# Kernel optimization log

Measured on AMD Instinct MI355X. Metric: run time of the kernel, lower is better.

The kernel has to match this reference:

```python
import jax, jax.numpy as jnp
import numpy as np

N_LINKS = 100000
N_EDGES = 1600000
D = 64          # link_state_dim
RU = 256        # readout_units
G = 256         # number of graphs
T = 4           # message passing iterations


def _glorot(key, shape):
    fan_in, fan_out = shape[0], shape[1]
    limit = np.sqrt(6.0 / (fan_in + fan_out)).astype(np.float32)
    return jax.random.uniform(key, shape, jnp.float32, -limit, limit)


def setup_inputs() -> dict:
    key = jax.random.key(0)
    ks = jax.random.split(key, 12)
    states_action = jax.random.normal(ks[0], (N_LINKS, D), jnp.float32)
    states_graph_ids = jnp.sort(jax.random.randint(ks[1], (N_LINKS,), 0, G))
    states_first = jax.random.randint(ks[2], (N_EDGES,), 0, N_LINKS)
    states_second = jax.random.randint(ks[3], (N_EDGES,), 0, N_LINKS)
    # Message: Dense(2D -> D) with selu
    W_msg = _glorot(ks[4], (2 * D, D)); b_msg = jnp.zeros((D,), jnp.float32)
    # GCN: Linear(D -> D) + relu, then unsorted_segment_sum
    W_gcn = _glorot(ks[5], (D, D)); b_gcn = jnp.zeros((D,), jnp.float32)
    # Readout MLP: D -> RU -> RU -> 1
    W_r1 = _glorot(ks[6], (D, RU)); b_r1 = jnp.zeros((RU,), jnp.float32)
    W_r2 = _glorot(ks[7], (RU, RU)); b_r2 = jnp.zeros((RU,), jnp.float32)
    W_r3 = _glorot(ks[8], (RU, 1)); b_r3 = jnp.zeros((1,), jnp.float32)
    return {
        "states_action": states_action,
        "W_msg": W_msg, "b_msg": b_msg,
        "W_gcn": W_gcn, "b_gcn": b_gcn,
        "W_r1": W_r1, "b_r1": b_r1,
        "W_r2": W_r2, "b_r2": b_r2,
        "W_r3": W_r3, "b_r3": b_r3,
        "states_graph_ids": states_graph_ids,
        "states_first": states_first,
        "states_second": states_second,
        "sates_num_edges": N_EDGES,
    }


def reference(states_action, W_msg, b_msg, W_gcn, b_gcn,
              W_r1, b_r1, W_r2, b_r2, W_r3, b_r3,
              states_graph_ids, states_first, states_second, sates_num_edges):
    n_links = states_action.shape[0]
    link_state = states_action
    for _ in range(T):
        main_e = link_state[states_first]      # [E, D]
        neigh_e = link_state[states_second]    # [E, D]
        concat = jnp.concatenate([main_e, neigh_e], axis=1)  # [E, 2D]
        msg = jax.nn.selu(concat @ W_msg + b_msg)            # [E, D]
        h = jax.nn.relu(msg @ W_gcn + b_gcn)                 # [E, D]
        # scatter-add messages back onto links (segment ids = states_second)
        link_state = jax.ops.segment_sum(h, states_second, num_segments=n_links)
        # dropout rate is 0.0 -> identity
    # per-graph readout (graph ids are sorted, fixed G segments)
    graph_emb = jax.ops.segment_sum(link_state, states_graph_ids, num_segments=G)
    r = jax.nn.selu(graph_emb @ W_r1 + b_r1)
    r = jax.nn.selu(r @ W_r2 + b_r2)
    r = r @ W_r3 + b_r3                                      # [G, 1]
    return r
```

## Files before the change

### kernel.cpp

```cpp
#include <hip/hip_runtime.h>
#include <hip/hip_bf16.h>
#include <math.h>

#define D 64
#define RU 256
#define CHUNK 8
#define QSTRIDE 68
#define SSTRIDE 72
#define BIN_SHIFT 7
#define NSB 256

#if __has_builtin(__builtin_amdgcn_exp2f)
#define EXP2F(x) __builtin_amdgcn_exp2f(x)
#else
#define EXP2F(x) exp2f(x)
#endif

typedef short bf16x8 __attribute__((ext_vector_type(8)));
typedef float f32x4 __attribute__((ext_vector_type(4)));

__device__ __forceinline__ float selu_f(float x) {
    return x > 0.0f ? 1.0507009873554805f * x
                    : 1.7580993408473766f * (__expf(x) - 1.0f);
}

__device__ __forceinline__ float selu_x2(float x2) {
    const float p = fmaxf(x2, 0.0f);
    const float n = fminf(x2, 0.0f);
    const float e = EXP2F(n);
    return fmaf(1.7580993408473766f, e, fmaf(0.72829042516f, p, -1.7580993408473766f));
}

__device__ __forceinline__ short f2bf_rtne(float x) {
    union { float f; unsigned u; } v; v.f = x;
    unsigned r = (v.u + 0x7FFFu + ((v.u >> 16) & 1u)) >> 16;
    return (short)r;
}
__device__ __forceinline__ float bf2f(short s) {
    union { float f; unsigned u; } v; v.u = ((unsigned)(unsigned short)s) << 16;
    return v.f;
}
__device__ __forceinline__ unsigned packpair(float a, float b) {
    float2 p; p.x = a; p.y = b;
    __hip_bfloat162 hb = __float22bfloat162_rn(p);
    return *(unsigned*)&hb;
}

__device__ __forceinline__ bf16x8 pack8(const float* v) {
    union { bf16x8 v; unsigned u[4]; } H;
#pragma unroll
    for (int j = 0; j < 4; ++j) H.u[j] = packpair(v[2 * j], v[2 * j + 1]);
    return H.v;
}

#define FIDX(ks, jt, qd, m) ((((((ks) * 4 + (jt)) * 4 + (qd)) * 16) + (m)) * 8)

__global__ __launch_bounds__(256) void wprep_kernel(
    const float* __restrict__ W_msg, const float* __restrict__ W_gcn,
    unsigned short* __restrict__ WAh, unsigned short* __restrict__ WAl,
    unsigned short* __restrict__ WBh, unsigned short* __restrict__ WBl,
    unsigned short* __restrict__ WGh)
{
    const float LOG2E = 1.4426950408889634f;
    const int t = blockIdx.x * 256 + threadIdx.x;
    if (t >= 4096) return;
    const int i  = t & 7;
    const int m  = (t >> 3) & 15;
    const int qd = (t >> 7) & 3;
    const int jt = (t >> 9) & 3;
    const int ks = t >> 11;
    const int kk = ks * 32 + qd * 8 + i;
    const int nn = jt * 16 + m;

    float w = W_msg[kk * 64 + nn] * LOG2E;
    short hi = f2bf_rtne(w);
    WAh[t] = (unsigned short)hi;
    WAl[t] = (unsigned short)f2bf_rtne(w - bf2f(hi));

    w = W_msg[(64 + kk) * 64 + nn] * LOG2E;
    hi = f2bf_rtne(w);
    WBh[t] = (unsigned short)hi;
    WBl[t] = (unsigned short)f2bf_rtne(w - bf2f(hi));

    WGh[t] = (unsigned short)f2bf_rtne(W_gcn[kk * 64 + nn]);
}

__global__ __launch_bounds__(256) void s2bf_kernel(
    const float* __restrict__ in, unsigned short* __restrict__ out, int n4)
{
    for (int i = blockIdx.x * 256 + threadIdx.x; i < n4; i += gridDim.x * 256) {
        const float4 v = ((const float4*)in)[i];
        uint2 o;
        o.x = packpair(v.x, v.y);
        o.y = packpair(v.z, v.w);
        ((uint2*)out)[i] = o;
    }
}


__global__ __launch_bounds__(256) void histA_kernel(
    const int* __restrict__ second, int* __restrict__ ghist,
    int n_edges, int nbins)
{
    __shared__ int lhist[1024];
    for (int i = threadIdx.x; i < nbins; i += 256) lhist[i] = 0;
    __syncthreads();
    const int per = (n_edges + gridDim.x - 1) / gridDim.x;
    const int e0 = blockIdx.x * per;
    const int e1 = min(e0 + per, n_edges);
    for (int e = e0 + threadIdx.x; e < e1; e += 256)
        atomicAdd(&lhist[second[e] >> BIN_SHIFT], 1);
    __syncthreads();
    for (int i = threadIdx.x; i < nbins; i += 256)
        ghist[i * gridDim.x + blockIdx.x] = lhist[i];
}

__global__ __launch_bounds__(64) void sumbins_kernel(
    int* __restrict__ ghist, int* __restrict__ btot, int nbins)
{
    const int b = blockIdx.x, tid = threadIdx.x;
    int d[4], p[4];
#pragma unroll
    for (int k = 0; k < 4; ++k) {
        d[k] = ghist[b * NSB + k * 64 + tid];
        p[k] = d[k];
    }
#pragma unroll
    for (int off = 1; off < 64; off <<= 1) {
#pragma unroll
        for (int k = 0; k < 4; ++k) {
            const int t = __shfl_up(p[k], off, 64);
            if (tid >= off) p[k] += t;
        }
    }
    int base = 0;
#pragma unroll
    for (int k = 0; k < 4; ++k) {
        const int tot = __shfl(p[k], 63, 64);
        ghist[b * NSB + k * 64 + tid] = base + p[k] - d[k];
        base += tot;
    }
    if (tid == 63) btot[b] = base;
}

__global__ __launch_bounds__(1024) void scanS_kernel(int* __restrict__ data, int n)
{
    __shared__ int wsum[16], woff[16];
    const int tid = threadIdx.x, wave = tid >> 6, lane = tid & 63;
    const int x = (tid < n) ? data[tid] : 0;
    int v = x;
#pragma unroll
    for (int off = 1; off < 64; off <<= 1) {
        const int t = __shfl_up(v, off, 64);
        if (lane >= off) v += t;
    }
    if (lane == 63) wsum[wave] = v;
    __syncthreads();
    if (wave == 0) {
        int s = (lane < 16) ? wsum[lane] : 0;
#pragma unroll
        for (int off = 1; off < 16; off <<= 1) {
            const int t = __shfl_up(s, off, 64);
            if (lane >= off) s += t;
        }
        if (lane < 16) woff[lane] = s - wsum[lane];
    }
    __syncthreads();
    if (tid < n) data[tid] = woff[wave] + v - x;
}

__global__ __launch_bounds__(256) void scatterC_kernel(
    const int* __restrict__ first, const int* __restrict__ second,
    const int* __restrict__ ghist, const int* __restrict__ btot,
    unsigned* __restrict__ tmp, int n_edges, int nbins)
{
    __shared__ int lcur[1024];
    for (int i = threadIdx.x; i < nbins; i += 256)
        lcur[i] = ghist[i * NSB + blockIdx.x] + btot[i];
    __syncthreads();
    const int per = (n_edges + gridDim.x - 1) / gridDim.x;
    const int e0 = blockIdx.x * per;
    const int e1 = min(e0 + per, n_edges);
    for (int e = e0 + threadIdx.x; e < e1; e += 256) {
        const int s = second[e];
        const int pos = atomicAdd(&lcur[s >> BIN_SHIFT], 1);
        tmp[pos] = (unsigned)first[e] | ((unsigned)(s & 127) << 20);
    }
}

__global__ __launch_bounds__(256) void binsortD_kernel(
    const unsigned* __restrict__ tmp, const int* __restrict__ btot,
    int* __restrict__ sfirst, int* __restrict__ row_ptr,
    int n_edges, int n_links, int nbins)
{
    __shared__ int ldeg[128];
    __shared__ int lpre[128];
    __shared__ int lcur[128];
    const int b = blockIdx.x;
    const int tid = threadIdx.x;
    const int lbase = b << BIN_SHIFT;
    const int nl = min(128, n_links - lbase);
    const int eb = btot[b];
    const int ee = (b + 1 < nbins) ? btot[b + 1] : n_edges;

    if (tid < 128) ldeg[tid] = 0;
    __syncthreads();
    for (int e = eb + tid; e < ee; e += 256)
        atomicAdd(&ldeg[tmp[e] >> 20], 1);
    __syncthreads();
    if (tid < 64) {
        const int d0 = ldeg[tid], d1 = ldeg[64 + tid];
        int p0 = d0, p1 = d1;
#pragma unroll
        for (int off = 1; off < 64; off <<= 1) {
            const int t0 = __shfl_up(p0, off, 64);
            const int t1 = __shfl_up(p1, off, 64);
            if (tid >= off) { p0 += t0; p1 += t1; }
        }
        const int tot0 = __shfl(p0, 63, 64);
        lpre[tid] = p0 - d0;
        lpre[64 + tid] = tot0 + p1 - d1;
    }
    __syncthreads();
    if (tid < nl) row_ptr[lbase + tid] = eb + lpre[tid];
    if (b == nbins - 1 && tid == 0) row_ptr[n_links] = n_edges;
    if (tid < 128) lcur[tid] = lpre[tid];
    __syncthreads();
    for (int e = eb + tid; e < ee; e += 256) {
        const unsigned v = tmp[e];
        const int pos = eb + atomicAdd(&lcur[v >> 20], 1);
        sfirst[pos] = (int)(v & 0x7FFFFFu);
    }
    if (b == 0)
        for (int i = tid; i < 64; i += 256) sfirst[n_edges + i] = 0;
}

__global__ __launch_bounds__(256) void growfind_kernel(
    const int* __restrict__ gid, int* __restrict__ grow, int n_links, int G)
{
    const int g = blockIdx.x * blockDim.x + threadIdx.x;
    if (g > G) return;
    if (g == G) { grow[G] = n_links; return; }
    int lo = 0, hi = n_links;
    while (lo < hi) {
        const int mid = (lo + hi) >> 1;
        if (gid[mid] < g) lo = mid + 1; else hi = mid;
    }
    grow[g] = lo;
}

__global__ __launch_bounds__(256) void p_mfma_kernel(
    const unsigned short* __restrict__ Sb,
    const unsigned short* __restrict__ WAh, const unsigned short* __restrict__ WAl,
    unsigned short* __restrict__ P, int n_links)
{
    const int tid = threadIdx.x;
    const int wave = tid >> 6;
    const int lane = tid & 63;
    const int m = lane & 15;
    const int qd = lane >> 4;

    bf16x8 Bh[2][4], Bl[2][4];
#pragma unroll
    for (int ks = 0; ks < 2; ++ks)
#pragma unroll
        for (int jt = 0; jt < 4; ++jt) {
            const int off = FIDX(ks, jt, qd, m);
            Bh[ks][jt] = *(const bf16x8*)(WAh + off);
            Bl[ks][jt] = *(const bf16x8*)(WAl + off);
        }
    const bf16x8 z = (bf16x8){0, 0, 0, 0, 0, 0, 0, 0};

    const int ngroups = (n_links + 63) >> 6;
    for (int g = blockIdx.x; g < ngroups; g += gridDim.x) {
        const int base = g * 64 + wave * 16;
        const int l = base + m;
        bf16x8 Ah0 = z, Ah1 = z;
        if (l < n_links) {
            Ah0 = *(const bf16x8*)(Sb + (size_t)l * D + qd * 8);
            Ah1 = *(const bf16x8*)(Sb + (size_t)l * D + 32 + qd * 8);
        }
        f32x4 accP[4];
#pragma unroll
        for (int jt = 0; jt < 4; ++jt) {
            accP[jt] = (f32x4){0.f, 0.f, 0.f, 0.f};
            accP[jt] = __builtin_amdgcn_mfma_f32_16x16x32_bf16(Ah0, Bh[0][jt], accP[jt], 0, 0, 0);
            accP[jt] = __builtin_amdgcn_mfma_f32_16x16x32_bf16(Ah0, Bl[0][jt], accP[jt], 0, 0, 0);
            accP[jt] = __builtin_amdgcn_mfma_f32_16x16x32_bf16(Ah1, Bh[1][jt], accP[jt], 0, 0, 0);
            accP[jt] = __builtin_amdgcn_mfma_f32_16x16x32_bf16(Ah1, Bl[1][jt], accP[jt], 0, 0, 0);
        }
#pragma unroll
        for (int r = 0; r < 4; ++r) {
            const int lr = base + qd * 4 + r;
            if (lr < n_links) {
#pragma unroll
                for (int jt = 0; jt < 4; ++jt)
                    P[(size_t)lr * D + jt * 16 + m] =
                        (unsigned short)f2bf_rtne(accP[jt][r]);
            }
        }
    }
}

__global__ __launch_bounds__(256, 4) void edge_link_kernel(
    unsigned short* __restrict__ Sb, const unsigned short* __restrict__ P,
    const int* __restrict__ sfirst, const int* __restrict__ row_ptr,
    const float* __restrict__ b_msg,
    const unsigned short* __restrict__ WBh, const unsigned short* __restrict__ WBl,
    const unsigned short* __restrict__ WGh,
    const float* __restrict__ b_gcn,
    const unsigned short* __restrict__ WAh, const unsigned short* __restrict__ WAl,
    unsigned short* __restrict__ Pout, int do_p,
    int n_links)
{
    __shared__ float qt[4][CHUNK * QSTRIDE + 4];
    __shared__ unsigned short srow[4][CHUNK * SSTRIDE];
    const int tid = threadIdx.x;
    const int wave = tid >> 6;
    const int lane = tid & 63;
    const int m = lane & 15;
    const int qd = lane >> 4;

    const int l0 = (blockIdx.x * 4 + wave) * CHUNK;
    if (l0 >= n_links) return;
    const int nl = min(CHUNK, n_links - l0);

    const float LOG2E = 1.4426950408889634f;
    float bmsgC[4];
#pragma unroll
    for (int jt = 0; jt < 4; ++jt) bmsgC[jt] = b_msg[jt * 16 + m] * LOG2E;

    {
        const bf16x8 z = (bf16x8){0, 0, 0, 0, 0, 0, 0, 0};
        const int l = l0 + m;
        bf16x8 Ah0 = z, Ah1 = z;
        if ((l < n_links) && (m < CHUNK)) {
            Ah0 = *(const bf16x8*)(Sb + (size_t)l * D + qd * 8);
            Ah1 = *(const bf16x8*)(Sb + (size_t)l * D + 32 + qd * 8);
        }
        f32x4 accQ[4];
#pragma unroll
        for (int jt = 0; jt < 4; ++jt) accQ[jt] = (f32x4){0.f, 0.f, 0.f, 0.f};
#pragma unroll
        for (int ks = 0; ks < 2; ++ks) {
            bf16x8 WbH[4], WbL[4];
#pragma unroll
            for (int jt = 0; jt < 4; ++jt) {
                const int off = FIDX(ks, jt, qd, m);
                WbH[jt] = *(const bf16x8*)(WBh + off);
                WbL[jt] = *(const bf16x8*)(WBl + off);
            }
            const bf16x8 A = ks ? Ah1 : Ah0;
#pragma unroll
            for (int jt = 0; jt < 4; ++jt) {
                accQ[jt] = __builtin_amdgcn_mfma_f32_16x16x32_bf16(A, WbH[jt], accQ[jt], 0, 0, 0);
                accQ[jt] = __builtin_amdgcn_mfma_f32_16x16x32_bf16(A, WbL[jt], accQ[jt], 0, 0, 0);
            }
        }
#pragma unroll
        for (int r = 0; r < 4; ++r) {
            const int row = qd * 4 + r;
            if (row < CHUNK) {
#pragma unroll
                for (int jt = 0; jt < 4; ++jt)
                    qt[wave][row * QSTRIDE + jt * 16 + m] = accQ[jt][r] + bmsgC[jt];
            }
        }
    }

    bf16x8 Gh[2][4];
#pragma unroll
    for (int ks = 0; ks < 2; ++ks)
#pragma unroll
        for (int jt = 0; jt < 4; ++jt)
            Gh[ks][jt] = *(const bf16x8*)(WGh + FIDX(ks, jt, qd, m));

    float bias_gcn[4];
#pragma unroll
    for (int jt = 0; jt < 4; ++jt) bias_gcn[jt] = b_gcn[jt * 16 + m];

    const int rpv = row_ptr[l0 + min(lane, nl)];
#define RP(i) __shfl(rpv, (i), 64)
    const int eb = __builtin_amdgcn_readfirstlane(RP(0));
    const int ee = __builtin_amdgcn_readfirstlane(RP(nl));
    if (eb >= ee) {
        for (int i = 0; i < nl; ++i) {
            Sb[(size_t)(l0 + i) * D + lane] = 0;
            if (do_p)
                __builtin_nontemporal_store((unsigned short)0,
                    &Pout[(size_t)(l0 + i) * D + lane]);
        }
        return;
    }
    const int ntiles = (ee - eb + 15) >> 4;

    int sv0 = sfirst[eb + m];
    int sv1 = sfirst[eb + 16 + m];
    bf16x8 p00, p01;
    {
        const unsigned short* Pr = P + (size_t)(sv0 & 0xFFFFF) * D;
        p00 = *(const bf16x8*)(Pr + qd * 8);
        p01 = *(const bf16x8*)(Pr + 32 + qd * 8);
    }

    int bcur = 0;
    float rsum[4] = {0.f, 0.f, 0.f, 0.f};
    int eo = eb;

    for (int t = 0; t < ntiles; ++t, eo += 16) {
        const int sv2 = sfirst[eo + 32 + m];
        const unsigned short* Pr1 = P + (size_t)(sv1 & 0xFFFFF) * D;
        const bf16x8 p10 = *(const bf16x8*)(Pr1 + qd * 8);
        const bf16x8 p11 = *(const bf16x8*)(Pr1 + 32 + qd * 8);

        const bool valid = (eo + m < ee);
        const int limv = valid ? ((sv0 >> 20) & 7) : 8;
        const int qoff = (valid ? ((sv0 >> 20) & 7) : 0) * QSTRIDE + qd * 8;

        float qb[16];
        *(float4*)&qb[0]  = *(const float4*)&qt[wave][qoff];
        *(float4*)&qb[4]  = *(const float4*)&qt[wave][qoff + 4];
        *(float4*)&qb[8]  = *(const float4*)&qt[wave][qoff + 32];
        *(float4*)&qb[12] = *(const float4*)&qt[wave][qoff + 36];

        float msgA[8];
#pragma unroll
        for (int i = 0; i < 8; ++i)
            msgA[i] = selu_x2(bf2f(p00[i]) + qb[i]);
        const bf16x8 Ah0 = pack8(msgA);
        float msgB[8];
#pragma unroll
        for (int i = 0; i < 8; ++i)
            msgB[i] = selu_x2(bf2f(p01[i]) + qb[8 + i]);
        const bf16x8 Ah1 = pack8(msgB);

        f32x4 acc[4];
#pragma unroll
        for (int jt = 0; jt < 4; ++jt) {
            const float b = bias_gcn[jt];
            acc[jt] = (f32x4){b, b, b, b};
            acc[jt] = __builtin_amdgcn_mfma_f32_16x16x32_bf16(Ah0, Gh[0][jt], acc[jt], 0, 0, 0);
            acc[jt] = __builtin_amdgcn_mfma_f32_16x16x32_bf16(Ah1, Gh[1][jt], acc[jt], 0, 0, 0);
        }

        float rel[4][4];
#pragma unroll
        for (int jt = 0; jt < 4; ++jt)
#pragma unroll
            for (int r = 0; r < 4; ++r)
                rel[jt][r] = fmaxf(acc[jt][r], 0.0f);

        const int lr0 = __shfl(limv, qd * 4 + 0, 64);
        const int lr1 = __shfl(limv, qd * 4 + 1, 64);
        const int lr2 = __shfl(limv, qd * 4 + 2, 64);
        const int lr3 = __shfl(limv, qd * 4 + 3, 64);

        while (true) {
            const int b0 = bcur;
#pragma unroll
            for (int jt = 0; jt < 4; ++jt) {
                rsum[jt] += ((lr0 == b0) ? rel[jt][0] : 0.0f)
                          + ((lr1 == b0) ? rel[jt][1] : 0.0f)
                          + ((lr2 == b0) ? rel[jt][2] : 0.0f)
                          + ((lr3 == b0) ? rel[jt][3] : 0.0f);
            }
            if (bcur < nl && RP(bcur + 1) <= eo + 16) {
#pragma unroll
                for (int jt = 0; jt < 4; ++jt) {
                    rsum[jt] += __shfl_xor(rsum[jt], 16, 64);
                    rsum[jt] += __shfl_xor(rsum[jt], 32, 64);
                }
                const float outv = (qd == 0) ? rsum[0] : (qd == 1) ? rsum[1]
                                 : (qd == 2) ? rsum[2] : rsum[3];
                const unsigned short sbv = (unsigned short)f2bf_rtne(outv);
                Sb[(size_t)(l0 + bcur) * D + lane] = sbv;
                srow[wave][bcur * SSTRIDE + lane] = sbv;
#pragma unroll
                for (int jt = 0; jt < 4; ++jt) rsum[jt] = 0.0f;
                ++bcur;
                if (bcur >= nl) break;
            } else {
                break;
            }
        }

        sv0 = sv1; sv1 = sv2;
        p00 = p10; p01 = p11;
    }

    while (bcur < nl) {
        Sb[(size_t)(l0 + bcur) * D + lane] = 0;
        srow[wave][bcur * SSTRIDE + lane] = 0;
        ++bcur;
    }

    if (do_p) {
        const bf16x8 z = (bf16x8){0, 0, 0, 0, 0, 0, 0, 0};
        bf16x8 Sa0 = z, Sa1 = z;
        if (m < nl) {
            Sa0 = *(const bf16x8*)&srow[wave][m * SSTRIDE + qd * 8];
            Sa1 = *(const bf16x8*)&srow[wave][m * SSTRIDE + 32 + qd * 8];
        }
        f32x4 accP[4];
#pragma unroll
        for (int jt = 0; jt < 4; ++jt) accP[jt] = (f32x4){0.f, 0.f, 0.f, 0.f};
#pragma unroll
        for (int ks = 0; ks < 2; ++ks) {
            const bf16x8 A = ks ? Sa1 : Sa0;
#pragma unroll
            for (int jt = 0; jt < 4; ++jt) {
                const int off = FIDX(ks, jt, qd, m);
                const bf16x8 BH = *(const bf16x8*)(WAh + off);
                const bf16x8 BL = *(const bf16x8*)(WAl + off);
                accP[jt] = __builtin_amdgcn_mfma_f32_16x16x32_bf16(A, BH, accP[jt], 0, 0, 0);
                accP[jt] = __builtin_amdgcn_mfma_f32_16x16x32_bf16(A, BL, accP[jt], 0, 0, 0);
            }
        }
#pragma unroll
        for (int r = 0; r < 4; ++r) {
            const int lr = qd * 4 + r;
            if (lr < nl) {
#pragma unroll
                for (int jt = 0; jt < 4; ++jt)
                    __builtin_nontemporal_store(
                        (unsigned short)f2bf_rtne(accP[jt][r]),
                        &Pout[(size_t)(l0 + lr) * D + jt * 16 + m]);
            }
        }
    }
#undef RP
}

__global__ __launch_bounds__(256) void gsum8_kernel(
    const unsigned short* __restrict__ Sb, const int* __restrict__ grow,
    float* __restrict__ gemb)
{
    __shared__ float red[4][64];
    const int g = blockIdx.x >> 3;
    const int slice = blockIdx.x & 7;
    const int slot = threadIdx.x >> 6;
    const int j = threadIdx.x & 63;
    const int ls = grow[g], le = grow[g + 1];
    float acc = 0.0f;
    for (int l = ls + slice * 4 + slot; l < le; l += 32)
        acc += bf2f((short)Sb[(size_t)l * D + j]);
    red[slot][j] = acc;
    __syncthreads();
    if (slot == 0)
        atomicAdd(&gemb[g * D + j], red[0][j] + red[1][j] + red[2][j] + red[3][j]);
}

__global__ __launch_bounds__(256) void mlp_kernel(
    const float* __restrict__ gemb,
    const float* __restrict__ W_r1, const float* __restrict__ b_r1,
    const float* __restrict__ W_r2, const float* __restrict__ b_r2,
    const float* __restrict__ W_r3, const float* __restrict__ b_r3,
    float* __restrict__ out)
{
    __shared__ float gl[64];
    __shared__ float row1[RU];
    __shared__ float row2[RU];
    __shared__ float fin[4];
    const int g = blockIdx.x;
    const int tid = threadIdx.x;
    const int slot = tid >> 6;
    const int lane = tid & 63;

    if (tid < 64) gl[tid] = gemb[g * D + tid];
    __syncthreads();

    float a1 = b_r1[tid];
#pragma unroll 8
    for (int k = 0; k < 64; ++k) a1 += gl[k] * W_r1[k * RU + tid];
    row1[tid] = selu_f(a1);
    __syncthreads();

    float a2 = b_r2[tid];
#pragma unroll 8
    for (int k = 0; k < RU; ++k) a2 += row1[k] * W_r2[k * RU + tid];
    row2[tid] = selu_f(a2);
    __syncthreads();

    float p = row2[tid] * W_r3[tid];
#pragma unroll
    for (int off = 32; off >= 1; off >>= 1)
        p += __shfl_down(p, off, 64);
    if (lane == 0) fin[slot] = p;
    __syncthreads();
    if (tid == 0)
        out[g] = fin[0] + fin[1] + fin[2] + fin[3] + b_r3[0];
}

extern "C" void kernel_launch(void* const* d_in, const int* in_sizes, int n_in,
                              void* d_out, int out_size, void* d_ws, size_t ws_size,
                              hipStream_t stream)
{
    const float* states_action = (const float*)d_in[0];
    const float* W_msg = (const float*)d_in[1];
    const float* b_msg = (const float*)d_in[2];
    const float* W_gcn = (const float*)d_in[3];
    const float* b_gcn = (const float*)d_in[4];
    const float* W_r1 = (const float*)d_in[5];
    const float* b_r1 = (const float*)d_in[6];
    const float* W_r2 = (const float*)d_in[7];
    const float* b_r2 = (const float*)d_in[8];
    const float* W_r3 = (const float*)d_in[9];
    const float* b_r3 = (const float*)d_in[10];
    const int* gid = (const int*)d_in[11];
    const int* first = (const int*)d_in[12];
    const int* second = (const int*)d_in[13];

    const int n_links = in_sizes[0] / D;
    const int n_edges = in_sizes[12];
    const int G = out_size;
    const int nbins = (n_links + 127) >> BIN_SHIFT;

    char* ws2 = (char*)d_ws;
    auto alloc = [&](size_t bytes) {
        char* p = ws2; ws2 += (bytes + 63) & ~(size_t)63; return p;
    };
    unsigned short* Sb = (unsigned short*)alloc((size_t)n_links * D * 2);
    unsigned short* Pb = (unsigned short*)alloc((size_t)n_links * D * 2);
    float* gemb = (float*)alloc((size_t)G * D * sizeof(float));
    int* row_ptr = (int*)alloc((size_t)(n_links + 1) * sizeof(int));
    int* grow = (int*)alloc((size_t)(G + 1) * sizeof(int));
    unsigned* tmp = (unsigned*)alloc((size_t)n_edges * sizeof(unsigned));
    int* sfirst = (int*)alloc((size_t)(n_edges + 64) * sizeof(int));
    unsigned short* WAh = (unsigned short*)alloc(4096 * 2);
    unsigned short* WAl = (unsigned short*)alloc(4096 * 2);
    unsigned short* WBh = (unsigned short*)alloc(4096 * 2);
    unsigned short* WBl = (unsigned short*)alloc(4096 * 2);
    unsigned short* WGh = (unsigned short*)alloc(4096 * 2);
    int* btot = (int*)alloc((size_t)nbins * sizeof(int));
    int* ghist = (int*)sfirst;

    const size_t used = (size_t)(ws2 - (char*)d_ws);
    const size_t p2bytes = (size_t)n_links * D * 2;
    const bool pfuse = (used + p2bytes + 64 <= ws_size);
    unsigned short* Pb2 = pfuse ? (unsigned short*)alloc(p2bytes) : Pb;

    hipMemsetAsync(gemb, 0, (size_t)G * D * sizeof(float), stream);
    s2bf_kernel<<<1024, 256, 0, stream>>>(states_action, Sb, n_links * D / 4);
    wprep_kernel<<<16, 256, 0, stream>>>(W_msg, W_gcn, WAh, WAl, WBh, WBl, WGh);
    histA_kernel<<<NSB, 256, 0, stream>>>(second, ghist, n_edges, nbins);
    sumbins_kernel<<<nbins, 64, 0, stream>>>(ghist, btot, nbins);
    scanS_kernel<<<1, 1024, 0, stream>>>(btot, nbins);
    scatterC_kernel<<<NSB, 256, 0, stream>>>(first, second, ghist, btot, tmp,
                                             n_edges, nbins);
    binsortD_kernel<<<nbins, 256, 0, stream>>>(tmp, btot, sfirst, row_ptr,
                                               n_edges, n_links, nbins);
    growfind_kernel<<<2, 256, 0, stream>>>(gid, grow, n_links, G);

    const int edge_blocks = (n_links + 4 * CHUNK - 1) / (4 * CHUNK);
    p_mfma_kernel<<<1024, 256, 0, stream>>>(Sb, WAh, WAl, Pb, n_links);
    if (pfuse) {
        unsigned short* Pc = Pb;
        unsigned short* Pn = Pb2;
        for (int t = 0; t < 4; ++t) {
            edge_link_kernel<<<edge_blocks, 256, 0, stream>>>(
                Sb, Pc, sfirst, row_ptr, b_msg, WBh, WBl, WGh, b_gcn,
                WAh, WAl, Pn, (t < 3) ? 1 : 0, n_links);
            unsigned short* sw = Pc; Pc = Pn; Pn = sw;
        }
    } else {
        for (int t = 0; t < 4; ++t) {
            if (t) p_mfma_kernel<<<1024, 256, 0, stream>>>(Sb, WAh, WAl, Pb, n_links);
            edge_link_kernel<<<edge_blocks, 256, 0, stream>>>(
                Sb, Pb, sfirst, row_ptr, b_msg, WBh, WBl, WGh, b_gcn,
                WAh, WAl, Pb, 0, n_links);
        }
    }

    gsum8_kernel<<<G * 8, 256, 0, stream>>>(Sb, grow, gemb);
    mlp_kernel<<<G, 256, 0, stream>>>(gemb, W_r1, b_r1, W_r2, b_r2,
                                      W_r3, b_r3, (float*)d_out);
}
```

Baseline: 449.8 us.

## Deepen gather prefetch, fold growfind and memset into wprep, relax occupancy

```diff
diff --git a/kernel.cpp b/kernel.cpp
--- a/kernel.cpp
+++ b/kernel.cpp
@@ -59,10 +59,28 @@
     const float* __restrict__ W_msg, const float* __restrict__ W_gcn,
     unsigned short* __restrict__ WAh, unsigned short* __restrict__ WAl,
     unsigned short* __restrict__ WBh, unsigned short* __restrict__ WBl,
-    unsigned short* __restrict__ WGh)
+    unsigned short* __restrict__ WGh,
+    float* __restrict__ gemb, const int* __restrict__ gid,
+    int* __restrict__ grow, int n_links, int G)
 {
     const float LOG2E = 1.4426950408889634f;
     const int t = blockIdx.x * 256 + threadIdx.x;
+
+    for (int i = t; i < G * 64; i += 16 * 256) gemb[i] = 0.0f;
+
+    if (t <= G) {
+        if (t == G) {
+            grow[G] = n_links;
+        } else {
+            int lo = 0, hi = n_links;
+            while (lo < hi) {
+                const int mid = (lo + hi) >> 1;
+                if (gid[mid] < t) lo = mid + 1; else hi = mid;
+            }
+            grow[t] = lo;
+        }
+    }
+
     if (t >= 4096) return;
     const int i  = t & 7;
     const int m  = (t >> 3) & 15;
@@ -73,14 +91,14 @@
     const int nn = jt * 16 + m;
 
     float w = W_msg[kk * 64 + nn] * LOG2E;
-    short hi = f2bf_rtne(w);
-    WAh[t] = (unsigned short)hi;
-    WAl[t] = (unsigned short)f2bf_rtne(w - bf2f(hi));
+    short hi2 = f2bf_rtne(w);
+    WAh[t] = (unsigned short)hi2;
+    WAl[t] = (unsigned short)f2bf_rtne(w - bf2f(hi2));
 
     w = W_msg[(64 + kk) * 64 + nn] * LOG2E;
-    hi = f2bf_rtne(w);
-    WBh[t] = (unsigned short)hi;
-    WBl[t] = (unsigned short)f2bf_rtne(w - bf2f(hi));
+    hi2 = f2bf_rtne(w);
+    WBh[t] = (unsigned short)hi2;
+    WBl[t] = (unsigned short)f2bf_rtne(w - bf2f(hi2));
 
     WGh[t] = (unsigned short)f2bf_rtne(W_gcn[kk * 64 + nn]);
 }
@@ -235,20 +253,6 @@
         for (int i = tid; i < 64; i += 256) sfirst[n_edges + i] = 0;
 }
 
-__global__ __launch_bounds__(256) void growfind_kernel(
-    const int* __restrict__ gid, int* __restrict__ grow, int n_links, int G)
-{
-    const int g = blockIdx.x * blockDim.x + threadIdx.x;
-    if (g > G) return;
-    if (g == G) { grow[G] = n_links; return; }
-    int lo = 0, hi = n_links;
-    while (lo < hi) {
-        const int mid = (lo + hi) >> 1;
-        if (gid[mid] < g) lo = mid + 1; else hi = mid;
-    }
-    grow[g] = lo;
-}
-
 __global__ __launch_bounds__(256) void p_mfma_kernel(
     const unsigned short* __restrict__ Sb,
     const unsigned short* __restrict__ WAh, const unsigned short* __restrict__ WAl,
@@ -302,7 +306,7 @@
     }
 }
 
-__global__ __launch_bounds__(256, 4) void edge_link_kernel(
+__global__ __launch_bounds__(256, 3) void edge_link_kernel(
     unsigned short* __restrict__ Sb, const unsigned short* __restrict__ P,
     const int* __restrict__ sfirst, const int* __restrict__ row_ptr,
     const float* __restrict__ b_msg,
@@ -386,9 +390,7 @@
     if (eb >= ee) {
         for (int i = 0; i < nl; ++i) {
             Sb[(size_t)(l0 + i) * D + lane] = 0;
-            if (do_p)
-                __builtin_nontemporal_store((unsigned short)0,
-                    &Pout[(size_t)(l0 + i) * D + lane]);
+            if (do_p) Pout[(size_t)(l0 + i) * D + lane] = 0;
         }
         return;
     }
@@ -396,11 +398,15 @@
 
     int sv0 = sfirst[eb + m];
     int sv1 = sfirst[eb + 16 + m];
-    bf16x8 p00, p01;
+    int sv2 = sfirst[eb + 32 + m];
+    bf16x8 p00, p01, p10, p11;
     {
         const unsigned short* Pr = P + (size_t)(sv0 & 0xFFFFF) * D;
         p00 = *(const bf16x8*)(Pr + qd * 8);
         p01 = *(const bf16x8*)(Pr + 32 + qd * 8);
+        const unsigned short* Pr1 = P + (size_t)(sv1 & 0xFFFFF) * D;
+        p10 = *(const bf16x8*)(Pr1 + qd * 8);
+        p11 = *(const bf16x8*)(Pr1 + 32 + qd * 8);
     }
 
     int bcur = 0;
@@ -408,10 +414,10 @@
     int eo = eb;
 
     for (int t = 0; t < ntiles; ++t, eo += 16) {
-        const int sv2 = sfirst[eo + 32 + m];
-        const unsigned short* Pr1 = P + (size_t)(sv1 & 0xFFFFF) * D;
-        const bf16x8 p10 = *(const bf16x8*)(Pr1 + qd * 8);
-        const bf16x8 p11 = *(const bf16x8*)(Pr1 + 32 + qd * 8);
+        const int sv3 = sfirst[eo + 48 + m];
+        const unsigned short* Pr2 = P + (size_t)(sv2 & 0xFFFFF) * D;
+        const bf16x8 p20 = *(const bf16x8*)(Pr2 + qd * 8);
+        const bf16x8 p21 = *(const bf16x8*)(Pr2 + 32 + qd * 8);
 
         const bool valid = (eo + m < ee);
         const int limv = valid ? ((sv0 >> 20) & 7) : 8;
@@ -484,8 +490,9 @@
             }
         }
 
-        sv0 = sv1; sv1 = sv2;
+        sv0 = sv1; sv1 = sv2; sv2 = sv3;
         p00 = p10; p01 = p11;
+        p10 = p20; p11 = p21;
     }
 
     while (bcur < nl) {
@@ -522,9 +529,8 @@
             if (lr < nl) {
 #pragma unroll
                 for (int jt = 0; jt < 4; ++jt)
-                    __builtin_nontemporal_store(
-                        (unsigned short)f2bf_rtne(accP[jt][r]),
-                        &Pout[(size_t)(l0 + lr) * D + jt * 16 + m]);
+                    Pout[(size_t)(l0 + lr) * D + jt * 16 + m] =
+                        (unsigned short)f2bf_rtne(accP[jt][r]);
             }
         }
     }
@@ -639,9 +645,9 @@
     const bool pfuse = (used + p2bytes + 64 <= ws_size);
     unsigned short* Pb2 = pfuse ? (unsigned short*)alloc(p2bytes) : Pb;
 
-    hipMemsetAsync(gemb, 0, (size_t)G * D * sizeof(float), stream);
     s2bf_kernel<<<1024, 256, 0, stream>>>(states_action, Sb, n_links * D / 4);
-    wprep_kernel<<<16, 256, 0, stream>>>(W_msg, W_gcn, WAh, WAl, WBh, WBl, WGh);
+    wprep_kernel<<<16, 256, 0, stream>>>(W_msg, W_gcn, WAh, WAl, WBh, WBl, WGh,
+                                         gemb, gid, grow, n_links, G);
     histA_kernel<<<NSB, 256, 0, stream>>>(second, ghist, n_edges, nbins);
     sumbins_kernel<<<nbins, 64, 0, stream>>>(ghist, btot, nbins);
     scanS_kernel<<<1, 1024, 0, stream>>>(btot, nbins);
@@ -649,7 +655,6 @@
                                              n_edges, nbins);
     binsortD_kernel<<<nbins, 256, 0, stream>>>(tmp, btot, sfirst, row_ptr,
                                                n_edges, n_links, nbins);
-    growfind_kernel<<<2, 256, 0, stream>>>(gid, grow, n_links, G);
 
     const int edge_blocks = (n_links + 4 * CHUNK - 1) / (4 * CHUNK);
     p_mfma_kernel<<<1024, 256, 0, stream>>>(Sb, WAh, WAl, Pb, n_links);
```

New measurement: 496.1 us. +10.3%, slower.
